# Performance work log

Hardware: AMD Instinct MI355X
Metric: run time of the kernel (lower is better)

The kernel has to match this reference:

```python
import math
import jax, jax.numpy as jnp
import numpy as np

# ---- static config (matches init_kwargs) ----
B, L, D = 32, 1024, 256
H = 4
E = D // H          # head dim = 64
LF = L // 2 + 1     # rfft bins = 513
LEFT, RIGHT = 205, 513   # retained freq band: int(LF*(1-0.6)) .. LF  (i=0, global mixer)
SPATIAL_RATIO = 0.1
TOP_K = int(5 * math.log(L))  # factor=5 -> 34
LN_EPS = 1e-8


def _layer_norm(x, g, b):
    m = jnp.mean(x, axis=-1, keepdims=True)
    v = jnp.mean((x - m) ** 2, axis=-1, keepdims=True)
    return (x - m) / jnp.sqrt(v + LN_EPS) * g + b


def _gelu_erf(x):
    return x * 0.5 * (1.0 + jax.lax.erf(x / math.sqrt(2.0)))


def _time_delay_agg_training(values, corr):
    # values, corr: [B,H,E,L]; shared top-k delay indices across batch (training path)
    mean_value = jnp.mean(corr, axis=(1, 2))                  # [B,L]
    _, index = jax.lax.top_k(jnp.mean(mean_value, axis=0), TOP_K)  # [TOP_K] int32
    weights = mean_value[:, index]                            # [B,TOP_K]
    tmp_corr = jax.nn.softmax(weights, axis=-1)               # [B,TOP_K]
    t = jnp.arange(L)

    def body(acc, args):
        idx, w = args                                         # idx: scalar delay, w: [B]
        pattern = jnp.take(values, (t + idx) % L, axis=-1)    # roll(values, -idx, axis=-1)
        return acc + pattern * w[:, None, None, None], None

    acc, _ = jax.lax.scan(body, jnp.zeros_like(values), (index, tmp_corr.T))
    return acc                                                # [B,H,E,L]


def setup_inputs() -> dict:
    key = jax.random.key(0)
    ks = jax.random.split(key, 12)
    lin = lambda k: jax.random.normal(k, (D, D), jnp.float32) * 0.02  # stored [in,out]
    return {
        "x": jax.random.normal(ks[0], (B, L, D), jnp.float32),
        "Wq": lin(ks[1]), "bq": jnp.zeros((D,), jnp.float32),
        "Wk": lin(ks[2]), "bk": jnp.zeros((D,), jnp.float32),
        "Wv": lin(ks[3]), "bv": jnp.zeros((D,), jnp.float32),
        "Wd": lin(ks[4]), "bd": jnp.zeros((D,), jnp.float32),
        "ln1_g": jnp.ones((D,), jnp.float32), "ln1_b": jnp.zeros((D,), jnp.float32),
        "W1": lin(ks[5]), "b1": jnp.zeros((D,), jnp.float32),
        "W2": lin(ks[6]), "b2": jnp.zeros((D,), jnp.float32),
        "ln2_g": jnp.ones((D,), jnp.float32), "ln2_b": jnp.zeros((D,), jnp.float32),
    }


def reference(x, Wq, bq, Wk, bk, Wv, bv, Wd, bd, ln1_g, ln1_b, W1, b1, W2, b2, ln2_g, ln2_b):
    # ---- HybridAttention ----
    q = (x @ Wq + bq).reshape(B, L, H, E).transpose(0, 2, 3, 1)  # [B,H,E,L]
    k = (x @ Wk + bk).reshape(B, L, H, E).transpose(0, 2, 3, 1)
    v = (x @ Wv + bv).reshape(B, L, H, E).transpose(0, 2, 3, 1)

    q_fft = jnp.fft.rfft(q, axis=-1)      # [B,H,E,LF]
    k_fft = jnp.fft.rfft(k, axis=-1)
    mask = jnp.zeros((LF,), jnp.float32).at[LEFT:RIGHT].set(1.0)

    # band-limited autocorrelation (equivalent to the index-box scatter/gather)
    corr = jnp.fft.irfft(q_fft * jnp.conj(k_fft) * mask, n=L, axis=-1)  # [B,H,E,L]
    Vt = _time_delay_agg_training(v, corr)                              # [B,H,E,L]
    context_time = Vt.transpose(0, 3, 1, 2).reshape(B, L, D)

    # spatial (band-pass filtered) attention branch
    v_fft = jnp.fft.rfft(v, axis=-1)
    qs = jnp.fft.irfft(q_fft * mask, n=L, axis=-1).transpose(0, 1, 3, 2)  # [B,H,L,E]
    ks_ = jnp.fft.irfft(k_fft * mask, n=L, axis=-1).transpose(0, 1, 3, 2)
    vs = jnp.fft.irfft(v_fft * mask, n=L, axis=-1).transpose(0, 1, 3, 2)
    scores = jnp.einsum('bhle,bhse->bhls', qs, ks_) / math.sqrt(E)
    probs = jax.nn.softmax(scores, axis=-1)
    ctx_sp = jnp.einsum('bhls,bhse->bhle', probs, vs).transpose(0, 2, 1, 3).reshape(B, L, D)

    context = (1.0 - SPATIAL_RATIO) * context_time + SPATIAL_RATIO * ctx_sp
    h = _layer_norm(context @ Wd + bd + x, ln1_g, ln1_b)

    # ---- FeedForward ----
    f = _gelu_erf(h @ W1 + b1) @ W2 + b2
    return _layer_norm(f + h, ln2_g, ln2_b)
```

## Files before the change

### kernel.cpp

```cpp
#include <hip/hip_runtime.h>
#include <hip/hip_bf16.h>
#include <math.h>

#define Lc 1024
#define Dc 256
#define Bc 32
#define Hc 4
#define Ec 64
#define TOPK 34
#define LEFTc 205

typedef unsigned short u16;
typedef __attribute__((ext_vector_type(8))) short bf16x8;
typedef __attribute__((ext_vector_type(4))) float f32x4;

__device__ __forceinline__ float bf2f(u16 u) {
    return __uint_as_float(((unsigned)u) << 16);
}
__device__ __forceinline__ u16 f2bf(float f) {
    unsigned u = __float_as_uint(f);
    u += 0x7FFFu + ((u >> 16) & 1u);
    return (u16)(u >> 16);
}

__global__ void detect_k(const u16* __restrict__ x, int* __restrict__ flag) {
    __shared__ int cnt;
    if (threadIdx.x == 0) cnt = 0;
    __syncthreads();
    int bad = 0;
    for (int i = threadIdx.x; i < 4096; i += 256) {
        float a = fabsf(bf2f(x[i]));
        if (!(a == 0.0f || (a >= 1e-8f && a <= 1e8f))) bad++;
    }
    atomicAdd(&cnt, bad);
    __syncthreads();
    if (threadIdx.x == 0) *flag = (cnt > 512) ? 1 : 0;
}

struct SrcPtrs { const void* p[17]; };
__global__ __launch_bounds__(256) void ingest_all_k(
    SrcPtrs sp, u16* __restrict__ cx, u16* __restrict__ wts, const int* __restrict__ flag)
{
    const long NB = (long)Bc * Lc * Dc;
    long i = (long)blockIdx.x * 256 + threadIdx.x;
    const int fp = *flag;
    const void* src; u16* dst; long off;
    if (i < NB) {
        src = sp.p[0]; dst = cx; off = i;
    } else {
        long j = i - NB;
        if (j < 6L * 65536) {
            const int w = (int)(j >> 16); off = j & 65535;
            const int wsidx[6] = {1, 3, 5, 7, 11, 13};
            src = sp.p[wsidx[w]]; dst = wts + (long)w * 65536;
        } else {
            long k2 = j - 6L * 65536;
            if (k2 >= 2560) return;
            const int v = (int)(k2 >> 8); off = k2 & 255;
            const int vsidx[10] = {2, 4, 6, 8, 9, 10, 12, 14, 15, 16};
            src = sp.p[vsidx[v]]; dst = wts + 6L * 65536 + (long)v * 256;
        }
    }
    dst[off] = fp ? f2bf(((const float*)src)[off]) : ((const u16*)src)[off];
}

__global__ void build_h(float* __restrict__ hf) {
    int d = blockIdx.x * blockDim.x + threadIdx.x;
    if (d >= Lc) return;
    float s = 0.f;
    for (int f = LEFTc; f < 512; ++f) {
        int m = (f * d) & (Lc - 1);
        s += __cosf((float)m * 6.135923151542565e-3f);
    }
    float ny = (d & 1) ? -1.f : 1.f;
    hf[d] = (2.f * s + ny) * (1.f / 1024.f);
}

__global__ void build_G(const float* __restrict__ hf, u16* __restrict__ G) {
    int i = blockIdx.x * 256 + threadIdx.x;
    int t = i >> 10, s = i & (Lc - 1);
    G[i] = f2bf(hf[(t - s) & (Lc - 1)]);
}

__global__ __launch_bounds__(256) void transpose_k(
    const u16* __restrict__ in, u16* __restrict__ out)
{
    __shared__ u16 t[32][33];
    const int l0 = blockIdx.x * 32, d0 = blockIdx.y * 32, b = blockIdx.z;
    const int tx = threadIdx.x & 31, ty = threadIdx.x >> 5;
    const u16* ib = in + (size_t)b * Lc * Dc;
    #pragma unroll
    for (int i = 0; i < 4; ++i)
        t[ty + i * 8][tx] = ib[(size_t)(l0 + ty + i * 8) * Dc + d0 + tx];
    __syncthreads();
    u16* ob = out + (size_t)b * Dc * Lc;
    #pragma unroll
    for (int i = 0; i < 4; ++i)
        ob[(size_t)(d0 + ty + i * 8) * Lc + l0 + tx] = t[tx][ty + i * 8];
}

__global__ __launch_bounds__(256) void wtrans_k(
    const u16* __restrict__ src, u16* __restrict__ dst)
{
    __shared__ u16 t[32][33];
    const int c0 = blockIdx.x * 32, r0 = blockIdx.y * 32;
    const u16* s = src + (size_t)blockIdx.z * 65536;
    u16* d = dst + (size_t)blockIdx.z * 65536;
    const int tx = threadIdx.x & 31, ty = threadIdx.x >> 5;
    #pragma unroll
    for (int i = 0; i < 4; ++i)
        t[ty + i * 8][tx] = s[(r0 + ty + i * 8) * 256 + c0 + tx];
    __syncthreads();
    #pragma unroll
    for (int i = 0; i < 4; ++i)
        d[(c0 + ty + i * 8) * 256 + r0 + tx] = t[tx][ty + i * 8];
}

template <int EPI, bool ACOMB>
__global__ __launch_bounds__(256) void mgemm_k(
    const u16* __restrict__ Abase, const u16* __restrict__ A2base,
    const u16* __restrict__ BTbase, const u16* __restrict__ bias,
    const u16* __restrict__ resid, u16* __restrict__ Cbase,
    int M, int N, int K, long strA, long strBT, long strC)
{
    const int z = blockIdx.z;
    const u16* A  = Abase + (size_t)z * strA;
    const u16* BT = BTbase + (size_t)z * strBT;
    u16* C        = Cbase + (size_t)z * strC;
    const int tid = threadIdx.x;
    const int wave = tid >> 6, lane = tid & 63;
    const int m16 = lane & 15, quad = lane >> 4;
    const int m0 = blockIdx.y * 128 + wave * 32;
    const int n0 = blockIdx.x * 64;

    __shared__ __align__(16) u16 sB[8192];

    const u16* arow0 = A + (size_t)(m0 + m16) * K + quad * 8;
    const u16* arow1 = arow0 + (size_t)16 * K;
    const u16* a2row0 = ACOMB ? (A2base + (size_t)z * strA + (size_t)(m0 + m16) * K + quad * 8) : nullptr;
    const u16* a2row1 = ACOMB ? (a2row0 + (size_t)16 * K) : nullptr;

    const u16* bgp[4];
    u16* bls[4];
    #pragma unroll
    for (int i = 0; i < 4; ++i) {
        const int c = tid + i * 256;
        const int nr = c >> 4, ko = c & 15;
        bgp[i] = BT + (size_t)(n0 + nr) * K + ko * 8;
        bls[i] = sB + ((nr >> 4) * 4 + (ko >> 2)) * 512 + (ko & 3) * 128
                    + (((nr & 15) ^ (ko & 3))) * 8;
    }

    bf16x8 breg[4];
    #pragma unroll
    for (int i = 0; i < 4; ++i) breg[i] = *(const bf16x8*)(bgp[i]);

    f32x4 acc[2][4] = {};

    #pragma unroll 1
    for (int kc = 0; kc < K; kc += 128) {
        #pragma unroll
        for (int i = 0; i < 4; ++i) *(bf16x8*)(bls[i]) = breg[i];
        __syncthreads();
        if (kc + 128 < K) {
            #pragma unroll
            for (int i = 0; i < 4; ++i) breg[i] = *(const bf16x8*)(bgp[i] + kc + 128);
        }
        #pragma unroll
        for (int kf = 0; kf < 4; ++kf) {
            bf16x8 a0 = *(const bf16x8*)(arow0 + kc + kf * 32);
            bf16x8 a1 = *(const bf16x8*)(arow1 + kc + kf * 32);
            if (ACOMB) {
                const bf16x8 x0 = *(const bf16x8*)(a2row0 + kc + kf * 32);
                const bf16x8 x1 = *(const bf16x8*)(a2row1 + kc + kf * 32);
                #pragma unroll
                for (int j = 0; j < 8; ++j) {
                    a0[j] = (short)f2bf(0.9f * bf2f((u16)a0[j]) + 0.1f * bf2f((u16)x0[j]));
                    a1[j] = (short)f2bf(0.9f * bf2f((u16)a1[j]) + 0.1f * bf2f((u16)x1[j]));
                }
            }
            #pragma unroll
            for (int nt = 0; nt < 4; ++nt) {
                const bf16x8 bf = *(const bf16x8*)(sB + (nt * 4 + kf) * 512 + quad * 128
                                                      + ((m16 ^ quad)) * 8);
                acc[0][nt] = __builtin_amdgcn_mfma_f32_16x16x32_bf16(a0, bf, acc[0][nt], 0, 0, 0);
                acc[1][nt] = __builtin_amdgcn_mfma_f32_16x16x32_bf16(a1, bf, acc[1][nt], 0, 0, 0);
            }
        }
        __syncthreads();
    }

    #pragma unroll
    for (int ms = 0; ms < 2; ++ms) {
        #pragma unroll
        for (int nt = 0; nt < 4; ++nt) {
            const int col = n0 + nt * 16 + m16;
            const float bv = bias ? bf2f(bias[col]) : 0.f;
            #pragma unroll
            for (int r = 0; r < 4; ++r) {
                const size_t off = (size_t)(m0 + ms * 16 + quad * 4 + r) * N + col;
                float v = acc[ms][nt][r] + bv;
                if (EPI == 1) v += bf2f(resid[off]);
                if (EPI == 2) v = 0.5f * v * (1.0f + erff(v * 0.70710678118654752f));
                C[off] = f2bf(v);
            }
        }
    }
}

__global__ __launch_bounds__(256) void corr_k(
    const u16* __restrict__ qs, const u16* __restrict__ ks, float* __restrict__ mv)
{
    const int l = blockIdx.x;
    const int b = ((l & 7) << 2) | ((l >> 3) & 3);
    const int rest = l >> 5;
    const int g = rest & 15;
    const int uq = rest >> 4;
    const int wave = threadIdx.x >> 6, lane = threadIdx.x & 63;
    const int m16 = lane & 15, quad = lane >> 4;
    const size_t base = (size_t)b * Lc * Dc;

    __shared__ float red[4][124];
    for (int i = threadIdx.x; i < 4 * 124; i += 256) ((float*)red)[i] = 0.f;
    __syncthreads();

    f32x4 acc[4] = {};
    #pragma unroll
    for (int ui = 0; ui < 4; ++ui) {
        const int u = uq * 16 + wave * 4 + ui;
        const u16* qrow = qs + base + (size_t)(u * 16 + m16) * Dc + quad * 8;
        const u16* kr[4];
        #pragma unroll
        for (int al = 0; al < 4; ++al) {
            const int s = (u - g * 4 - al) & 63;
            kr[al] = ks + base + (size_t)(s * 16 + m16) * Dc + quad * 8;
        }
        #pragma unroll
        for (int k0 = 0; k0 < Dc; k0 += 32) {
            const bf16x8 aq = *(const bf16x8*)(qrow + k0);
            #pragma unroll
            for (int al = 0; al < 4; ++al) {
                const bf16x8 bk = *(const bf16x8*)(kr[al] + k0);
                acc[al] = __builtin_amdgcn_mfma_f32_16x16x32_bf16(aq, bk, acc[al], 0, 0, 0);
            }
        }
    }

    #pragma unroll
    for (int al = 0; al < 4; ++al)
        #pragma unroll
        for (int r = 0; r < 4; ++r)
            atomicAdd(&red[wave][al * 31 + quad * 4 + r - m16 + 15], acc[al][r]);
    __syncthreads();

    if (threadIdx.x < 124) {
        const int al = threadIdx.x / 31, dd = threadIdx.x % 31;
        const float s = red[0][threadIdx.x] + red[1][threadIdx.x] +
                        red[2][threadIdx.x] + red[3][threadIdx.x];
        atomicAdd(&mv[b * Lc + (((g * 4 + al) * 16 + dd - 15) & (Lc - 1))], s);
    }
}

__global__ __launch_bounds__(256) void attn_k(
    const u16* __restrict__ qs, const u16* __restrict__ ks,
    const u16* __restrict__ vsT, u16* __restrict__ ctx)
{
    const int lt = blockIdx.x, h = blockIdx.y, b = blockIdx.z;

    __shared__ __align__(16) u16 sK[8192];
    __shared__ __align__(16) u16 sV[8192];
    __shared__ __align__(16) u16 sP[8192];

    const int tid  = threadIdx.x;
    const int wave = tid >> 6;
    const int lane = tid & 63;
    const int m16  = lane & 15;
    const int quad = lane >> 4;
    const int l0   = lt * 64;
    const size_t base = (size_t)b * Lc * Dc + (size_t)h * Ec;
    const size_t vtbase = ((size_t)b * Dc + (size_t)h * Ec) * Lc;

    const u16* qrow = qs + base + (size_t)(l0 + wave * 16 + m16) * Dc + quad * 8;
    const bf16x8 qa0 = *(const bf16x8*)(qrow);
    const bf16x8 qa1 = *(const bf16x8*)(qrow + 32);

    const u16* kgp[4]; const u16* vgp[4];
    u16* kls[4]; u16* vls[4];
    #pragma unroll
    for (int i = 0; i < 4; ++i) {
        const int c = tid + i * 256;
        const int sr = c >> 3, eo = c & 7;
        kgp[i] = ks + base + (size_t)sr * Dc + eo * 8;
        kls[i] = sK + ((sr >> 4) * 2 + (eo >> 2)) * 512 + (eo & 3) * 128
                    + (((sr & 15) ^ (eo & 3))) * 8;
        const int er = c >> 4, so = c & 15;
        vgp[i] = vsT + vtbase + (size_t)er * Lc + so * 8;
        vls[i] = sV + ((er >> 4) * 4 + (so >> 2)) * 512 + (so & 3) * 128
                    + (((er & 15) ^ (so & 3))) * 8;
    }

    bf16x8 kreg[4], vreg[4];
    #pragma unroll
    for (int i = 0; i < 4; ++i) {
        kreg[i] = *(const bf16x8*)(kgp[i]);
        vreg[i] = *(const bf16x8*)(vgp[i]);
    }

    f32x4 o[4] = {};
    float rs[4] = {0.f, 0.f, 0.f, 0.f};

    const int rsw = m16 ^ quad;
    const int hrd = ((quad & 1) << 1) | (m16 >> 3);
    const int prd = (m16 ^ hrd) * 8;

    #pragma unroll 1
    for (int s0 = 0; s0 < Lc; s0 += 128) {
        #pragma unroll
        for (int i = 0; i < 4; ++i) {
            *(bf16x8*)(kls[i]) = kreg[i];
            *(bf16x8*)(vls[i]) = vreg[i];
        }
        __syncthreads();
        if (s0 + 128 < Lc) {
            #pragma unroll
            for (int i = 0; i < 4; ++i) {
                kreg[i] = *(const bf16x8*)(kgp[i] + (size_t)(s0 + 128) * Dc);
                vreg[i] = *(const bf16x8*)(vgp[i] + (s0 + 128));
            }
        }

        #pragma unroll
        for (int st = 0; st < 8; ++st) {
            const bf16x8 kb0 = *(const bf16x8*)(sK + (st * 2 + 0) * 512 + quad * 128 + rsw * 8);
            const bf16x8 kb1 = *(const bf16x8*)(sK + (st * 2 + 1) * 512 + quad * 128 + rsw * 8);
            f32x4 c4 = {0.f, 0.f, 0.f, 0.f};
            c4 = __builtin_amdgcn_mfma_f32_16x16x32_bf16(qa0, kb0, c4, 0, 0, 0);
            c4 = __builtin_amdgcn_mfma_f32_16x16x32_bf16(qa1, kb1, c4, 0, 0, 0);
            const int q2 = ((st & 1) << 1) | (m16 >> 3);
            const int hst = ((q2 & 1) << 1) | (quad >> 1);
            u16* pw = sP + wave * 2048 + (st >> 1) * 512 + q2 * 128 + (m16 & 7);
            #pragma unroll
            for (int r = 0; r < 4; ++r) {
                const float p = __expf(c4[r] * 0.125f);
                rs[r] += p;
                pw[(((quad * 4 + r) ^ hst)) * 8] = f2bf(p);
            }
        }
        __syncthreads();

        const bf16x8 a0 = *(const bf16x8*)(sP + wave * 2048 + 0 * 512 + quad * 128 + prd);
        const bf16x8 a1 = *(const bf16x8*)(sP + wave * 2048 + 1 * 512 + quad * 128 + prd);
        const bf16x8 a2 = *(const bf16x8*)(sP + wave * 2048 + 2 * 512 + quad * 128 + prd);
        const bf16x8 a3 = *(const bf16x8*)(sP + wave * 2048 + 3 * 512 + quad * 128 + prd);
        #pragma unroll
        for (int nt = 0; nt < 4; ++nt) {
            o[nt] = __builtin_amdgcn_mfma_f32_16x16x32_bf16(a0, *(const bf16x8*)(sV + (nt * 4 + 0) * 512 + quad * 128 + rsw * 8), o[nt], 0, 0, 0);
            o[nt] = __builtin_amdgcn_mfma_f32_16x16x32_bf16(a1, *(const bf16x8*)(sV + (nt * 4 + 1) * 512 + quad * 128 + rsw * 8), o[nt], 0, 0, 0);
            o[nt] = __builtin_amdgcn_mfma_f32_16x16x32_bf16(a2, *(const bf16x8*)(sV + (nt * 4 + 2) * 512 + quad * 128 + rsw * 8), o[nt], 0, 0, 0);
            o[nt] = __builtin_amdgcn_mfma_f32_16x16x32_bf16(a3, *(const bf16x8*)(sV + (nt * 4 + 3) * 512 + quad * 128 + rsw * 8), o[nt], 0, 0, 0);
        }
        __syncthreads();
    }

    #pragma unroll
    for (int off = 1; off < 16; off <<= 1) {
        #pragma unroll
        for (int r = 0; r < 4; ++r) rs[r] += __shfl_xor(rs[r], off);
    }
    #pragma unroll
    for (int nt = 0; nt < 4; ++nt) {
        #pragma unroll
        for (int r = 0; r < 4; ++r)
            ctx[base + (size_t)(l0 + wave * 16 + quad * 4 + r) * Dc + nt * 16 + m16] =
                f2bf(o[nt][r] / rs[r]);
    }
}

__global__ __launch_bounds__(1024) void topk_k(
    const float* __restrict__ mv, int* __restrict__ idx_g, float* __restrict__ w_g)
{
    __shared__ float wvs[16];
    __shared__ int   wis[16];
    __shared__ int   widx;
    __shared__ int   sidx[TOPK];
    const int tid = threadIdx.x;
    const int lane = tid & 63;
    const int wv_id = tid >> 6;

    float g = 0.f;
    for (int b = 0; b < Bc; ++b) g += mv[b * Lc + tid];

    for (int j = 0; j < TOPK; ++j) {
        float v = g; int ix = tid;
        #pragma unroll
        for (int off = 32; off > 0; off >>= 1) {
            const float ov = __shfl_xor(v, off);
            const int   oi = __shfl_xor(ix, off);
            if (ov > v || (ov == v && oi < ix)) { v = ov; ix = oi; }
        }
        if (lane == 0) { wvs[wv_id] = v; wis[wv_id] = ix; }
        __syncthreads();
        if (tid == 0) {
            float bv = wvs[0]; int bi = wis[0];
            for (int u = 1; u < 16; ++u)
                if (wvs[u] > bv || (wvs[u] == bv && wis[u] < bi)) { bv = wvs[u]; bi = wis[u]; }
            widx = bi; sidx[j] = bi; idx_g[j] = bi;
        }
        __syncthreads();
        if (tid == widx) g = -3e38f;
        __syncthreads();
    }
    if (tid < Bc) {
        float wv[TOPK];
        float mx = -3e38f;
        for (int j = 0; j < TOPK; ++j) {
            wv[j] = mv[tid * Lc + sidx[j]] * (1.0f / (float)Dc);
            mx = fmaxf(mx, wv[j]);
        }
        float sum = 0.f;
        for (int j = 0; j < TOPK; ++j) { wv[j] = expf(wv[j] - mx); sum += wv[j]; }
        for (int j = 0; j < TOPK; ++j) w_g[tid * TOPK + j] = wv[j] / sum;
    }
}

__global__ __launch_bounds__(256) void agg_k(
    const u16* __restrict__ v, const int* __restrict__ idx,
    const float* __restrict__ w, u16* __restrict__ ct)
{
    const int b = blockIdx.y;
    const int t = blockIdx.x * 4 + (threadIdx.x >> 6);
    const int lane = threadIdx.x & 63;
    __shared__ int   sidx[TOPK];
    __shared__ float sw[TOPK];
    if (threadIdx.x < TOPK) { sidx[threadIdx.x] = idx[threadIdx.x]; sw[threadIdx.x] = w[b * TOPK + threadIdx.x]; }
    __syncthreads();
    const u16* vb = v + (size_t)b * Lc * Dc;
    const int c4 = lane * 4;
    float a0 = 0.f, a1 = 0.f, a2 = 0.f, a3 = 0.f;
    for (int j = 0; j < TOPK; ++j) {
        const float wj = sw[j];
        const ushort4 u = *reinterpret_cast<const ushort4*>(
            vb + (size_t)((t + sidx[j]) & (Lc - 1)) * Dc + c4);
        a0 += wj * bf2f(u.x); a1 += wj * bf2f(u.y);
        a2 += wj * bf2f(u.z); a3 += wj * bf2f(u.w);
    }
    ushort4 o; o.x = f2bf(a0); o.y = f2bf(a1); o.z = f2bf(a2); o.w = f2bf(a3);
    *reinterpret_cast<ushort4*>(ct + (size_t)b * Lc * Dc + (size_t)t * Dc + c4) = o;
}

template <bool FINAL>
__global__ __launch_bounds__(256) void ln_k(
    const u16* __restrict__ in, const u16* __restrict__ g,
    const u16* __restrict__ be, void* __restrict__ out, const int* __restrict__ flag)
{
    const int wave = threadIdx.x >> 6, lane = threadIdx.x & 63;
    const int row = blockIdx.x * 4 + wave;
    const int c4 = lane * 4;
    const ushort4 u = *reinterpret_cast<const ushort4*>(in + (size_t)row * Dc + c4);
    float x[4] = {bf2f(u.x), bf2f(u.y), bf2f(u.z), bf2f(u.w)};
    float sm = x[0] + x[1] + x[2] + x[3];
    float sq = x[0]*x[0] + x[1]*x[1] + x[2]*x[2] + x[3]*x[3];
    #pragma unroll
    for (int off = 1; off < 64; off <<= 1) {
        sm += __shfl_xor(sm, off);
        sq += __shfl_xor(sq, off);
    }
    const float mean = sm * (1.f / 256.f);
    const float var = sq * (1.f / 256.f) - mean * mean;
    const float rstd = __frsqrt_rn(var + 1e-8f);
    const ushort4 gg = *reinterpret_cast<const ushort4*>(g + c4);
    const ushort4 bb = *reinterpret_cast<const ushort4*>(be + c4);
    float y[4];
    y[0] = (x[0] - mean) * rstd * bf2f(gg.x) + bf2f(bb.x);
    y[1] = (x[1] - mean) * rstd * bf2f(gg.y) + bf2f(bb.y);
    y[2] = (x[2] - mean) * rstd * bf2f(gg.z) + bf2f(bb.z);
    y[3] = (x[3] - mean) * rstd * bf2f(gg.w) + bf2f(bb.w);
    if (FINAL && *flag) {
        float4 o = make_float4(y[0], y[1], y[2], y[3]);
        *reinterpret_cast<float4*>((float*)out + (size_t)row * Dc + c4) = o;
    } else {
        ushort4 o; o.x = f2bf(y[0]); o.y = f2bf(y[1]); o.z = f2bf(y[2]); o.w = f2bf(y[3]);
        *reinterpret_cast<ushort4*>((u16*)out + (size_t)row * Dc + c4) = o;
    }
}

extern "C" void kernel_launch(void* const* d_in, const int* in_sizes, int n_in,
                              void* d_out, int out_size, void* d_ws, size_t ws_size,
                              hipStream_t stream)
{
    (void)in_sizes; (void)n_in; (void)out_size; (void)ws_size;

    const size_t BLD = (size_t)Bc * Lc * Dc;
    const size_t SLOT = BLD * 2;
    const long LD = (long)(Lc * Dc);
    char* ws = (char*)d_ws;
    u16* b0 = (u16*)(ws + 0 * SLOT);
    u16* b1 = (u16*)(ws + 1 * SLOT);
    u16* b2 = (u16*)(ws + 2 * SLOT);
    u16* b3 = (u16*)(ws + 3 * SLOT);
    u16* cx = (u16*)(ws + 4 * SLOT);
    u16* G  = (u16*)(ws + 5 * SLOT);
    char* tail = ws + 5 * SLOT + (size_t)Lc * Lc * 2;
    u16* wts  = (u16*)tail;
    u16* wtsT = wts + 6 * 65536 + 10 * 256;
    char* tail2 = (char*)(wtsT + 6 * 65536);
    float* hf  = (float*)(tail2 + 512);
    float* mv  = hf + Lc;
    int*   idx = (int*)(mv + Bc * Lc);
    float* wsm = (float*)(idx + 64);
    int*   flag = (int*)(wsm + Bc * TOPK);

    u16* vecs = wts + 6 * 65536;
    u16* cbv = vecs + 2 * 256;  u16* cbd = vecs + 3 * 256;
    u16* l1g = vecs + 4 * 256;  u16* l1b = vecs + 5 * 256;
    u16* cb1 = vecs + 6 * 256;  u16* cb2 = vecs + 7 * 256;
    u16* l2g = vecs + 8 * 256;  u16* l2b = vecs + 9 * 256;
    u16* wvT = wtsT + 2 * 65536;
    u16* wdT = wtsT + 3 * 65536; u16* w1T = wtsT + 4 * 65536; u16* w2T = wtsT + 5 * 65536;

    detect_k<<<dim3(1), 256, 0, stream>>>((const u16*)d_in[0], flag);
    SrcPtrs sp;
    for (int i = 0; i < 17; ++i) sp.p[i] = d_in[i];
    ingest_all_k<<<dim3(34314), 256, 0, stream>>>(sp, cx, wts, flag);
    wtrans_k<<<dim3(8, 8, 6), 256, 0, stream>>>(wts, wtsT);

    build_h<<<dim3(4), 256, 0, stream>>>(hf);
    build_G<<<dim3((Lc * Lc) / 256), 256, 0, stream>>>(hf, G);

    transpose_k<<<dim3(32, 8, 32), 256, 0, stream>>>(cx, b1);
    mgemm_k<0, false><<<dim3(4, 8, 32), 256, 0, stream>>>(
        G, nullptr, b1, nullptr, nullptr, b0, Lc, Dc, Lc, 0, LD, LD);

    mgemm_k<0, false><<<dim3(4, 256, 3), 256, 0, stream>>>(
        b0, nullptr, wtsT, nullptr, nullptr, b1, Bc * Lc, Dc, Dc, 0, 65536, (long)BLD);

    hipMemsetAsync(mv, 0, (size_t)Bc * Lc * 4, stream);
    corr_k<<<dim3(2048), 256, 0, stream>>>(b1, b2, mv);

    transpose_k<<<dim3(32, 8, 32), 256, 0, stream>>>(b3, b0);
    attn_k<<<dim3(16, 4, 32), 256, 0, stream>>>(b1, b2, b0, b3);

    topk_k<<<dim3(1), 1024, 0, stream>>>(mv, idx, wsm);

    const dim3 gProj(4, 256, 1);
    mgemm_k<0, false><<<gProj, 256, 0, stream>>>(cx, nullptr, wvT, cbv, nullptr, b1, Bc * Lc, Dc, Dc, 0, 0, 0);
    agg_k<<<dim3(256, 32), 256, 0, stream>>>(b1, idx, wsm, b2);

    mgemm_k<1, true><<<gProj, 256, 0, stream>>>(b2, b3, wdT, cbd, cx, b0, Bc * Lc, Dc, Dc, 0, 0, 0);

    ln_k<false><<<dim3(8192), 256, 0, stream>>>(b0, l1g, l1b, b1, flag);

    mgemm_k<2, false><<<gProj, 256, 0, stream>>>(b1, nullptr, w1T, cb1, nullptr, b2, Bc * Lc, Dc, Dc, 0, 0, 0);
    mgemm_k<1, false><<<gProj, 256, 0, stream>>>(b2, nullptr, w2T, cb2, b1, b3, Bc * Lc, Dc, Dc, 0, 0, 0);

    ln_k<true><<<dim3(8192), 256, 0, stream>>>(b3, l2g, l2b, d_out, flag);
}
```

Measured before the change: 621.1 us.

## Retile correlation kernel as LDS-staged 128x64 GEMM with diagonal-binned reduction

The correlation kernel is restructured from per-wave diagonal tile groups that read Q and K straight from global memory into a conventional per-batch GEMM tile. Each block covers 128 query rows by 64 key rows. K rows are staged through a swizzled LDS buffer with register prefetch of the next K chunk, and each wave reuses two A fragments across four B fragments. Diagonal sums are binned into a 191-entry shared array and then atomically added to the per-batch lag vector. This is meant to raise data reuse and cut redundant global and L2 traffic. In exchange it uses more blocks, more LDS atomics and slightly more global atomics per block.

```diff
diff --git a/kernel.cpp b/kernel.cpp
--- a/kernel.cpp
+++ b/kernel.cpp
@@ -211,54 +211,81 @@
 __global__ __launch_bounds__(256) void corr_k(
     const u16* __restrict__ qs, const u16* __restrict__ ks, float* __restrict__ mv)
 {
-    const int l = blockIdx.x;
-    const int b = ((l & 7) << 2) | ((l >> 3) & 3);
-    const int rest = l >> 5;
-    const int g = rest & 15;
-    const int uq = rest >> 4;
-    const int wave = threadIdx.x >> 6, lane = threadIdx.x & 63;
+    const int b = blockIdx.z;
+    const u16* A  = qs + (size_t)b * Lc * Dc;
+    const u16* BT = ks + (size_t)b * Lc * Dc;
+    const int tid = threadIdx.x;
+    const int wave = tid >> 6, lane = tid & 63;
     const int m16 = lane & 15, quad = lane >> 4;
-    const size_t base = (size_t)b * Lc * Dc;
-
-    __shared__ float red[4][124];
-    for (int i = threadIdx.x; i < 4 * 124; i += 256) ((float*)red)[i] = 0.f;
+    const int m0 = blockIdx.y * 128 + wave * 32;
+    const int n0 = blockIdx.x * 64;
+    const int K = Dc;
+
+    __shared__ __align__(16) u16 sB[8192];
+    __shared__ float red[191];
+
+    for (int i = tid; i < 191; i += 256) red[i] = 0.f;
+
+    const u16* arow0 = A + (size_t)(m0 + m16) * K + quad * 8;
+    const u16* arow1 = arow0 + (size_t)16 * K;
+
+    const u16* bgp[4];
+    u16* bls[4];
+    #pragma unroll
+    for (int i = 0; i < 4; ++i) {
+        const int c = tid + i * 256;
+        const int nr = c >> 4, ko = c & 15;
+        bgp[i] = BT + (size_t)(n0 + nr) * K + ko * 8;
+        bls[i] = sB + ((nr >> 4) * 4 + (ko >> 2)) * 512 + (ko & 3) * 128
+                    + (((nr & 15) ^ (ko & 3))) * 8;
+    }
+
+    bf16x8 breg[4];
+    #pragma unroll
+    for (int i = 0; i < 4; ++i) breg[i] = *(const bf16x8*)(bgp[i]);
+
+    f32x4 acc[2][4] = {};
+
+    #pragma unroll 1
+    for (int kc = 0; kc < K; kc += 128) {
+        #pragma unroll
+        for (int i = 0; i < 4; ++i) *(bf16x8*)(bls[i]) = breg[i];
+        __syncthreads();
+        if (kc + 128 < K) {
+            #pragma unroll
+            for (int i = 0; i < 4; ++i) breg[i] = *(const bf16x8*)(bgp[i] + kc + 128);
+        }
+        #pragma unroll
+        for (int kf = 0; kf < 4; ++kf) {
+            const bf16x8 a0 = *(const bf16x8*)(arow0 + kc + kf * 32);
+            const bf16x8 a1 = *(const bf16x8*)(arow1 + kc + kf * 32);
+            #pragma unroll
+            for (int nt = 0; nt < 4; ++nt) {
+                const bf16x8 bf = *(const bf16x8*)(sB + (nt * 4 + kf) * 512 + quad * 128
+                                                      + ((m16 ^ quad)) * 8);
+                acc[0][nt] = __builtin_amdgcn_mfma_f32_16x16x32_bf16(a0, bf, acc[0][nt], 0, 0, 0);
+                acc[1][nt] = __builtin_amdgcn_mfma_f32_16x16x32_bf16(a1, bf, acc[1][nt], 0, 0, 0);
+            }
+        }
+        __syncthreads();
+    }
+
+    #pragma unroll
+    for (int ms = 0; ms < 2; ++ms) {
+        #pragma unroll
+        for (int nt = 0; nt < 4; ++nt) {
+            const int binb = (wave * 32 + ms * 16 + quad * 4) - (nt * 16 + m16) + 63;
+            #pragma unroll
+            for (int r = 0; r < 4; ++r)
+                unsafeAtomicAdd(&red[binb + r], acc[ms][nt][r]);
+        }
+    }
     __syncthreads();
 
-    f32x4 acc[4] = {};
-    #pragma unroll
-    for (int ui = 0; ui < 4; ++ui) {
-        const int u = uq * 16 + wave * 4 + ui;
-        const u16* qrow = qs + base + (size_t)(u * 16 + m16) * Dc + quad * 8;
-        const u16* kr[4];
-        #pragma unroll
-        for (int al = 0; al < 4; ++al) {
-            const int s = (u - g * 4 - al) & 63;
-            kr[al] = ks + base + (size_t)(s * 16 + m16) * Dc + quad * 8;
-        }
-        #pragma unroll
-        for (int k0 = 0; k0 < Dc; k0 += 32) {
-            const bf16x8 aq = *(const bf16x8*)(qrow + k0);
-            #pragma unroll
-            for (int al = 0; al < 4; ++al) {
-                const bf16x8 bk = *(const bf16x8*)(kr[al] + k0);
-                acc[al] = __builtin_amdgcn_mfma_f32_16x16x32_bf16(aq, bk, acc[al], 0, 0, 0);
-            }
-        }
-    }
-
-    #pragma unroll
-    for (int al = 0; al < 4; ++al)
-        #pragma unroll
-        for (int r = 0; r < 4; ++r)
-            atomicAdd(&red[wave][al * 31 + quad * 4 + r - m16 + 15], acc[al][r]);
-    __syncthreads();
-
-    if (threadIdx.x < 124) {
-        const int al = threadIdx.x / 31, dd = threadIdx.x % 31;
-        const float s = red[0][threadIdx.x] + red[1][threadIdx.x] +
-                        red[2][threadIdx.x] + red[3][threadIdx.x];
-        atomicAdd(&mv[b * Lc + (((g * 4 + al) * 16 + dd - 15) & (Lc - 1))], s);
-    }
+    float* mvb = mv + (size_t)b * Lc;
+    const int tb = blockIdx.y * 128 - n0 - 63;
+    for (int i = tid; i < 191; i += 256)
+        unsafeAtomicAdd(&mvb[(tb + i) & (Lc - 1)], red[i]);
 }
 
 __global__ __launch_bounds__(256) void attn_k(
@@ -535,7 +562,7 @@
         b0, nullptr, wtsT, nullptr, nullptr, b1, Bc * Lc, Dc, Dc, 0, 65536, (long)BLD);
 
     hipMemsetAsync(mv, 0, (size_t)Bc * Lc * 4, stream);
-    corr_k<<<dim3(2048), 256, 0, stream>>>(b1, b2, mv);
+    corr_k<<<dim3(16, 8, 32), 256, 0, stream>>>(b1, b2, mv);
 
     transpose_k<<<dim3(32, 8, 32), 256, 0, stream>>>(b3, b0);
     attn_k<<<dim3(16, 4, 32), 256, 0, stream>>>(b1, b2, b0, b3);
```

Result: slower. 714.1 us (+15.0%).
